# Kernel tuning notes

Measured on AMD Instinct MI355X. Metric: run time of the kernel, lower is better.

## Reference

```python
import jax, jax.numpy as jnp
import numpy as np

HIDDEN = 512
NUM_HEADS = 8
HEAD = HIDDEN // NUM_HEADS
TOP_K = 64
NEG = -1e9


def setup_inputs() -> dict:
    key = jax.random.key(0)
    ks = jax.random.split(key, 12)
    B, Q, S = 2, 2048, 4096
    sc = 0.02
    return {
        "main_input": jax.random.normal(ks[0], (B, Q, HIDDEN), jnp.float32),
        "side_input": jax.random.normal(ks[1], (S, HIDDEN), jnp.float32),
        "att_mask": jax.random.randint(ks[2], (B, Q, S), 0, 2, jnp.int32),
        "Wq": jax.random.normal(ks[3], (HIDDEN, HIDDEN), jnp.float32) * sc,
        "bq": jnp.zeros((HIDDEN,), jnp.float32),
        "Wk": jax.random.normal(ks[4], (HIDDEN, HIDDEN), jnp.float32) * sc,
        "bk": jnp.zeros((HIDDEN,), jnp.float32),
        "Wv": jax.random.normal(ks[5], (HIDDEN, HIDDEN), jnp.float32) * sc,
        "bv": jnp.zeros((HIDDEN,), jnp.float32),
        "Wo": jax.random.normal(ks[6], (HIDDEN, HIDDEN), jnp.float32) * sc,
        "bo": jnp.zeros((HIDDEN,), jnp.float32),
    }


def reference(main_input, side_input, att_mask, Wq, bq, Wk, bk, Wv, bv, Wo, bo):
    B, Qlen, _ = main_input.shape
    S = side_input.shape[0]
    # multi-head projections; side K/V shared across the whole batch
    q = (main_input @ Wq + bq).reshape(B, Qlen, NUM_HEADS, HEAD)
    k = (side_input @ Wk + bk).reshape(S, NUM_HEADS, HEAD)
    v = (side_input @ Wv + bv).reshape(S, NUM_HEADS, HEAD)
    # scores: [B, H, Q, S]
    scores = jnp.einsum("bqhd,khd->bhqk", q, k) / jnp.sqrt(jnp.asarray(HEAD, q.dtype))
    # attention mask (0 = masked)
    mask = att_mask[:, None, :, :].astype(scores.dtype)  # [B,1,Q,S]
    scores = scores + (1.0 - mask) * NEG
    # top-k restriction: keep only the TOP_K largest scores per query row
    thresh = jax.lax.top_k(scores, TOP_K)[0][..., -1:]  # kth largest
    scores = jnp.where(scores >= thresh, scores, NEG)
    probs = jax.nn.softmax(scores, axis=-1)
    ctx = jnp.einsum("bhqk,khd->bqhd", probs, v).reshape(B, Qlen, HIDDEN)
    return ctx @ Wo + bo
```

## Files before the change

### kernel.cpp

```cpp
#include <hip/hip_runtime.h>
#include <stdint.h>

typedef uint32_t u32;
typedef unsigned long long u64;

#define NEGV (-1e9f)
#define NCAND 16
#define LISTCAP 256

__device__ __forceinline__ u32 f2ord(float f) {
  u32 x = __float_as_uint(f);
  return (x & 0x80000000u) ? ~x : (x | 0x80000000u);
}
__device__ __forceinline__ float ord2f(u32 u) {
  u32 x = (u & 0x80000000u) ? (u ^ 0x80000000u) : ~u;
  return __uint_as_float(x);
}

__global__ __launch_bounds__(256)
void pack_mask(const int* __restrict__ mask, u64* __restrict__ mbits) {
  int w = blockIdx.x * 256 + threadIdx.x;
  const int4* p = (const int4*)(mask + (size_t)w * 64);
  u64 bits = 0;
#pragma unroll
  for (int j = 0; j < 16; ++j) {
    int4 m = p[j];
    if (m.x) bits |= 1ull << (j * 4 + 0);
    if (m.y) bits |= 1ull << (j * 4 + 1);
    if (m.z) bits |= 1ull << (j * 4 + 2);
    if (m.w) bits |= 1ull << (j * 4 + 3);
  }
  mbits[w] = bits;
}

__global__ __launch_bounds__(256)
void gemm_bias(const float* __restrict__ A, const float* __restrict__ W,
               const float* __restrict__ bias, float* __restrict__ C) {
  __shared__ float As[16][68];
  __shared__ float Bs[16][64];
  const int tid = threadIdx.x;
  const int tx = tid & 15, ty = tid >> 4;
  const int n0 = blockIdx.x << 6, m0 = blockIdx.y << 6;
  float c[4][4] = {};
  for (int k0 = 0; k0 < 512; k0 += 16) {
    {
      const int row = tid >> 2, kp = (tid & 3) << 2;
      float4 av = *(const float4*)&A[(size_t)(m0 + row) * 512 + k0 + kp];
      As[kp + 0][row] = av.x;
      As[kp + 1][row] = av.y;
      As[kp + 2][row] = av.z;
      As[kp + 3][row] = av.w;
      const int kk = tid >> 4, np = (tid & 15) << 2;
      *(float4*)&Bs[kk][np] = *(const float4*)&W[(size_t)(k0 + kk) * 512 + n0 + np];
    }
    __syncthreads();
#pragma unroll
    for (int kk = 0; kk < 16; ++kk) {
      float4 a = *(const float4*)&As[kk][ty << 2];
      float4 b = *(const float4*)&Bs[kk][tx << 2];
      c[0][0] += a.x * b.x; c[0][1] += a.x * b.y; c[0][2] += a.x * b.z; c[0][3] += a.x * b.w;
      c[1][0] += a.y * b.x; c[1][1] += a.y * b.y; c[1][2] += a.y * b.z; c[1][3] += a.y * b.w;
      c[2][0] += a.z * b.x; c[2][1] += a.z * b.y; c[2][2] += a.z * b.z; c[2][3] += a.z * b.w;
      c[3][0] += a.w * b.x; c[3][1] += a.w * b.y; c[3][2] += a.w * b.z; c[3][3] += a.w * b.w;
    }
    __syncthreads();
  }
  float4 bv = *(const float4*)&bias[n0 + (tx << 2)];
#pragma unroll
  for (int i = 0; i < 4; ++i) {
    float4 o;
    o.x = c[i][0] + bv.x; o.y = c[i][1] + bv.y;
    o.z = c[i][2] + bv.z; o.w = c[i][3] + bv.w;
    *(float4*)&C[(size_t)(m0 + (ty << 2) + i) * 512 + n0 + (tx << 2)] = o;
  }
}

__global__ __launch_bounds__(256)
void gemm_bias_T(const float* __restrict__ A, const float* __restrict__ W,
                 const float* __restrict__ bias, float* __restrict__ CT, int qsh) {
  __shared__ float As[16][68];
  __shared__ float Bs[16][64];
  const int tid = threadIdx.x;
  const int tx = tid & 15, ty = tid >> 4;
  const int n0 = blockIdx.x << 6, m0 = blockIdx.y << 6;
  float c[4][4] = {};
  for (int k0 = 0; k0 < 512; k0 += 16) {
    {
      const int row = tid >> 2, kp = (tid & 3) << 2;
      float4 av = *(const float4*)&A[(size_t)(m0 + row) * 512 + k0 + kp];
      As[kp + 0][row] = av.x;
      As[kp + 1][row] = av.y;
      As[kp + 2][row] = av.z;
      As[kp + 3][row] = av.w;
      const int kk = tid >> 4, np = (tid & 15) << 2;
      *(float4*)&Bs[kk][np] = *(const float4*)&W[(size_t)(k0 + kk) * 512 + n0 + np];
    }
    __syncthreads();
#pragma unroll
    for (int kk = 0; kk < 16; ++kk) {
      float4 a = *(const float4*)&As[kk][ty << 2];
      float4 b = *(const float4*)&Bs[kk][tx << 2];
      c[0][0] += a.x * b.x; c[0][1] += a.x * b.y; c[0][2] += a.x * b.z; c[0][3] += a.x * b.w;
      c[1][0] += a.y * b.x; c[1][1] += a.y * b.y; c[1][2] += a.y * b.z; c[1][3] += a.y * b.w;
      c[2][0] += a.z * b.x; c[2][1] += a.z * b.y; c[2][2] += a.z * b.z; c[2][3] += a.z * b.w;
      c[3][0] += a.w * b.x; c[3][1] += a.w * b.y; c[3][2] += a.w * b.z; c[3][3] += a.w * b.w;
    }
    __syncthreads();
  }
  float4 bv = *(const float4*)&bias[n0 + (tx << 2)];
  float bvv[4] = {bv.x, bv.y, bv.z, bv.w};
  const int qlen = 1 << qsh;
  const int qmask = qlen - 1;
#pragma unroll
  for (int i = 0; i < 4; ++i) {
#pragma unroll
    for (int j = 0; j < 4; ++j) {
      float val = c[i][j] + bvv[j];
      int m = m0 + (ty << 2) + i;
      int n = n0 + (tx << 2) + j;
      int h = n >> 6, d = n & 63;
      int bb = m >> qsh, q = m & qmask;
      CT[(((size_t)bb * 8 + h) * 64 + d) * qlen + q] = val;
    }
  }
}

__global__ __launch_bounds__(256)
void score_kernel(const float* __restrict__ qT, const float* __restrict__ kT,
                  const u64* __restrict__ mbits, float* __restrict__ sbuf,
                  float* __restrict__ segmax, int sl0) {
  __shared__ float Qs[64][128];
  __shared__ float Ks[64][128];
  const int sl = sl0 + blockIdx.z;
  const int b = sl >> 3, h = sl & 7;
  const int s0 = blockIdx.x << 7, q0 = blockIdx.y << 7;
  const int tid = threadIdx.x;
  const float* qbase = qT + (size_t)sl * 64 * 2048 + q0;
  const float* kbase = kT + (size_t)h * 64 * 4096 + s0;
  float4* Qf = (float4*)&Qs[0][0];
  float4* Kf = (float4*)&Ks[0][0];
#pragma unroll
  for (int u = 0; u < 8; ++u) {
    int i = (u << 8) + tid;
    int row = i >> 5, col = (i & 31) << 2;
    Qf[i] = *(const float4*)(qbase + (size_t)row * 2048 + col);
    Kf[i] = *(const float4*)(kbase + (size_t)row * 4096 + col);
  }
  __syncthreads();
  const int tx = tid & 15, ty = tid >> 4;
  float c[8][8] = {};
#pragma unroll 4
  for (int g = 0; g < 16; ++g) {
    const int kk = g << 2;
    float qa[8][4], kb[8][4];
#pragma unroll
    for (int t = 0; t < 4; ++t) {
#pragma unroll
      for (int i = 0; i < 8; ++i) qa[i][t] = Qs[kk + t][(ty << 3) + i];
#pragma unroll
      for (int j = 0; j < 4; ++j) {
        kb[j][t]     = Ks[kk + t][(tx << 2) + j];
        kb[4 + j][t] = Ks[kk + t][64 + (tx << 2) + j];
      }
    }
#pragma unroll
    for (int i = 0; i < 8; ++i)
#pragma unroll
      for (int j = 0; j < 8; ++j)
        c[i][j] += qa[i][0] * kb[j][0] + qa[i][1] * kb[j][1]
                 + qa[i][2] * kb[j][2] + qa[i][3] * kb[j][3];
  }
  float* srow = sbuf + ((size_t)blockIdx.z * 2048 + q0) * 4096 + s0;
  const u64* mrow = mbits + ((size_t)(b * 2048 + q0)) * 64 + (s0 >> 6);
#pragma unroll
  for (int i = 0; i < 8; ++i) {
    const int row = (ty << 3) + i;
    u64 wA = mrow[(size_t)row * 64];
    u64 wB = mrow[(size_t)row * 64 + 1];
    float4 o0, o1;
    o0.x = ((wA >> ((tx << 2) + 0)) & 1) ? c[i][0] * 0.125f : NEGV;
    o0.y = ((wA >> ((tx << 2) + 1)) & 1) ? c[i][1] * 0.125f : NEGV;
    o0.z = ((wA >> ((tx << 2) + 2)) & 1) ? c[i][2] * 0.125f : NEGV;
    o0.w = ((wA >> ((tx << 2) + 3)) & 1) ? c[i][3] * 0.125f : NEGV;
    o1.x = ((wB >> ((tx << 2) + 0)) & 1) ? c[i][4] * 0.125f : NEGV;
    o1.y = ((wB >> ((tx << 2) + 1)) & 1) ? c[i][5] * 0.125f : NEGV;
    o1.z = ((wB >> ((tx << 2) + 2)) & 1) ? c[i][6] * 0.125f : NEGV;
    o1.w = ((wB >> ((tx << 2) + 3)) & 1) ? c[i][7] * 0.125f : NEGV;
    *(float4*)&srow[(size_t)row * 4096 + (tx << 2)] = o0;
    *(float4*)&srow[(size_t)row * 4096 + 64 + (tx << 2)] = o1;
    float m0 = fmaxf(fmaxf(o0.x, o0.y), fmaxf(o0.z, o0.w));
    float m1 = fmaxf(fmaxf(o1.x, o1.y), fmaxf(o1.z, o1.w));
#pragma unroll
    for (int off = 4; off; off >>= 1) {
      m0 = fmaxf(m0, __shfl_xor(m0, off, 64));
      m1 = fmaxf(m1, __shfl_xor(m1, off, 64));
    }
    if ((tx & 7) == 0) {
      size_t sg = ((size_t)blockIdx.z * 2048 + q0 + row) * 128 + (s0 >> 5) + (tx >> 3);
      segmax[sg] = m0;
      segmax[sg + 2] = m1;
    }
  }
}

__global__ __launch_bounds__(256)
void topk_ctx_kernel(const float* __restrict__ sbuf, const float* __restrict__ segmax,
                     const float* __restrict__ vbuf, float* __restrict__ ctxbuf,
                     int sl0) {
  const int sl = sl0 + blockIdx.y;
  const int b = sl >> 3, h = sl & 7;
  const int w = threadIdx.x >> 6, lane = threadIdx.x & 63;
  const int qi = (blockIdx.x << 2) + w;
  __shared__ u64 cand_lds[4][NCAND][64];
  u64* list = &cand_lds[w][0][0];
  const u64 lmask_lt = (1ull << lane) - 1ull;
  const u32 ordneg = f2ord(NEGV);

  const float* srow = sbuf + ((size_t)blockIdx.y * 2048 + qi) * 4096;

  float2 smv = *(const float2*)(segmax + ((size_t)blockIdx.y * 2048 + qi) * 128 + (lane << 1));
  u32 so0 = f2ord(smv.x), so1 = f2ord(smv.y);
  u32 mxo = so0 > so1 ? so0 : so1;
  u32 mno = so0 < so1 ? so0 : so1;
#pragma unroll
  for (int off = 32; off; off >>= 1) {
    u32 a = (u32)__shfl_xor((int)mxo, off, 64);
    u32 c = (u32)__shfl_xor((int)mno, off, 64);
    mxo = a > mxo ? a : mxo;
    mno = c < mno ? c : mno;
  }
  const float fm = ord2f(mxo);
  {
    u32 lo = mno, hi = mxo + 1;
    while (hi - lo > 1) {
      u32 mid = lo + ((hi - lo) >> 1);
      int c = __popcll(__ballot(so0 >= mid)) + __popcll(__ballot(so1 >= mid));
      if (c >= 64) lo = mid; else hi = mid;
    }
    mno = lo;
  }
  const u32 ordT = mno;
  const float Tf = ord2f(ordT);

  int cnt = 0;
  const float* lbase = srow + (lane << 6);
#pragma unroll
  for (int reg = 0; reg < 2; ++reg) {
    bool active = (reg == 0) ? (smv.x >= Tf) : (smv.y >= Tf);
    if (active) {
      const float* rb = lbase + (reg << 5);
      float4 v0 = *(const float4*)(rb + 0);
      float4 v1 = *(const float4*)(rb + 4);
      float4 v2 = *(const float4*)(rb + 8);
      float4 v3 = *(const float4*)(rb + 12);
      float4 v4 = *(const float4*)(rb + 16);
      float4 v5 = *(const float4*)(rb + 20);
      float4 v6 = *(const float4*)(rb + 24);
      float4 v7 = *(const float4*)(rb + 28);
      float xs[32] = {v0.x, v0.y, v0.z, v0.w, v1.x, v1.y, v1.z, v1.w,
                      v2.x, v2.y, v2.z, v2.w, v3.x, v3.y, v3.z, v3.w,
                      v4.x, v4.y, v4.z, v4.w, v5.x, v5.y, v5.z, v5.w,
                      v6.x, v6.y, v6.z, v6.w, v7.x, v7.y, v7.z, v7.w};
#pragma unroll
      for (int cc = 0; cc < 32; ++cc) {
        if (xs[cc] >= Tf) {
          if (cnt < NCAND) {
            int sidx = (lane << 6) + (reg << 5) + cc;
            cand_lds[w][cnt][lane] = ((u64)f2ord(xs[cc]) << 32) | (u32)sidx;
          }
          cnt++;
        }
      }
    }
  }
  const bool fb = (__ballot(cnt > NCAND) != 0ull);

  float esum = 0.f;
  int nsel = 0;
  bool meanpath = false;

  if (!fb) {
    u32 co[NCAND];
#pragma unroll
    for (int j = 0; j < NCAND; ++j)
      co[j] = (j < cnt) ? ((const u32*)&cand_lds[w][j][lane])[1] : 0u;
    u32 lo = ordT, hi = mxo + 1;
    while (hi - lo > 1) {
      u32 mid = lo + ((hi - lo) >> 1);
      int c = 0;
#pragma unroll
      for (int j = 0; j < NCAND; ++j)
        c += __popcll(__ballot(co[j] >= mid));
      if (c >= 64) lo = mid; else hi = mid;
    }
    int base = 0;
#pragma unroll
    for (int j = 0; j < NCAND; ++j) {
      bool pred = (j < cnt) && (co[j] >= lo);
      u64 m = __ballot(pred);
      int ofs = base + __popcll(m & lmask_lt);
      if (pred && ofs < LISTCAP) {
        u64 cj = cand_lds[w][j][lane];
        float ev = __expf(ord2f((u32)(cj >> 32)) - fm);
        list[ofs] = ((u64)((u32)cj) << 32) | (u64)__float_as_uint(ev);
        esum += ev;
      }
      base += (int)__popcll(m);
    }
    nsel = base < LISTCAP ? base : LISTCAP;
  } else {
    u32 lo = ordT, hi = mxo + 1;
    while (hi - lo > 1) {
      u32 mid = lo + ((hi - lo) >> 1);
      float midf = ord2f(mid);
      int c = 0;
      for (int j = 0; j < 16; ++j) {
        float4 v = *(const float4*)(srow + (j << 8) + (lane << 2));
        c += __popcll(__ballot(v.x >= midf)) + __popcll(__ballot(v.y >= midf)) +
             __popcll(__ballot(v.z >= midf)) + __popcll(__ballot(v.w >= midf));
      }
      if (c >= 64) lo = mid; else hi = mid;
    }
    const float thrf = ord2f(lo);
    int base = 0;
    for (int j = 0; j < 16; ++j) {
      float4 v = *(const float4*)(srow + (j << 8) + (lane << 2));
      float xs[4] = {v.x, v.y, v.z, v.w};
#pragma unroll
      for (int cpos = 0; cpos < 4; ++cpos) {
        float x = xs[cpos];
        bool pred = (x >= thrf) && (x != NEGV);
        u64 m = __ballot(pred);
        int ofs = base + __popcll(m & lmask_lt);
        if (pred && ofs < LISTCAP) {
          int sidx = (j << 8) + (lane << 2) + cpos;
          float ev = __expf(x - fm);
          list[ofs] = ((u64)(u32)sidx << 32) | (u64)__float_as_uint(ev);
          esum += ev;
        }
        base += (int)__popcll(m);
      }
    }
    nsel = base < LISTCAP ? base : LISTCAP;
    if (base == 0) meanpath = true;
  }

#pragma unroll
  for (int off = 32; off; off >>= 1) esum += __shfl_xor(esum, off, 64);
  const float* vb = vbuf + h * 64 + lane;
  float outv;
  if (!meanpath) {
    const float rs = 1.0f / esum;
    int pad = (8 - (nsel & 7)) & 7;
    if (lane < pad && nsel + lane < LISTCAP) list[nsel + lane] = 0;
    int n8 = nsel + pad;
    if (n8 > LISTCAP) n8 = LISTCAP;
    float a0 = 0.f, a1 = 0.f, a2 = 0.f, a3 = 0.f;
    float a4 = 0.f, a5 = 0.f, a6 = 0.f, a7 = 0.f;
    for (int g = 0; g < n8; g += 8) {
      u64 p0 = list[g + 0], p1 = list[g + 1], p2 = list[g + 2], p3 = list[g + 3];
      u64 p4 = list[g + 4], p5 = list[g + 5], p6 = list[g + 6], p7 = list[g + 7];
      a0 += __uint_as_float((u32)p0) * vb[(size_t)(p0 >> 32) * 512];
      a1 += __uint_as_float((u32)p1) * vb[(size_t)(p1 >> 32) * 512];
      a2 += __uint_as_float((u32)p2) * vb[(size_t)(p2 >> 32) * 512];
      a3 += __uint_as_float((u32)p3) * vb[(size_t)(p3 >> 32) * 512];
      a4 += __uint_as_float((u32)p4) * vb[(size_t)(p4 >> 32) * 512];
      a5 += __uint_as_float((u32)p5) * vb[(size_t)(p5 >> 32) * 512];
      a6 += __uint_as_float((u32)p6) * vb[(size_t)(p6 >> 32) * 512];
      a7 += __uint_as_float((u32)p7) * vb[(size_t)(p7 >> 32) * 512];
    }
    outv = (((a0 + a1) + (a2 + a3)) + ((a4 + a5) + (a6 + a7))) * rs;
  } else {
    float acc = 0.f;
    for (int s = 0; s < 4096; ++s) acc += vb[(size_t)s * 512];
    outv = acc * (1.0f / 4096.0f);
  }
  ctxbuf[((size_t)(b * 2048 + qi)) * 512 + h * 64 + lane] = outv;
}

extern "C" void kernel_launch(void* const* d_in, const int* in_sizes, int n_in,
                              void* d_out, int out_size, void* d_ws, size_t ws_size,
                              hipStream_t stream) {
  const float* main_in = (const float*)d_in[0];
  const float* side_in = (const float*)d_in[1];
  const int*   mask    = (const int*)d_in[2];
  const float* Wq = (const float*)d_in[3];
  const float* bq = (const float*)d_in[4];
  const float* Wk = (const float*)d_in[5];
  const float* bk = (const float*)d_in[6];
  const float* Wv = (const float*)d_in[7];
  const float* bv = (const float*)d_in[8];
  const float* Wo = (const float*)d_in[9];
  const float* bo = (const float*)d_in[10];
  float* out = (float*)d_out;

  char* ws = (char*)d_ws;
  float* qT   = (float*)(ws);
  float* kT   = (float*)(ws + ((size_t)8 << 20));
  float* vbuf = (float*)(ws + ((size_t)16 << 20));
  float* ctxb = (float*)(ws + ((size_t)24 << 20));
  u64* mbits  = (u64*)(ws + ((size_t)32 << 20));
  const size_t base = (size_t)34 << 20;
  const size_t sliceb = (size_t)2048 * 4096 * 4;
  const size_t segb   = (size_t)2048 * 128 * 4;
  const size_t per = sliceb + segb;

  int nz = 1;
  if (ws_size > base + per) {
    size_t m = (ws_size - base) / per;
    nz = (int)(m > 4 ? 4 : m);
  }
  float* sbuf = (float*)(ws + base);
  float* smax = (float*)(ws + base + (size_t)nz * sliceb);

  pack_mask<<<1024, 256, 0, stream>>>(mask, mbits);
  gemm_bias_T<<<dim3(8, 64), 256, 0, stream>>>(main_in, Wq, bq, qT, 11);
  gemm_bias_T<<<dim3(8, 64), 256, 0, stream>>>(side_in, Wk, bk, kT, 12);
  gemm_bias  <<<dim3(8, 64), 256, 0, stream>>>(side_in, Wv, bv, vbuf);

  for (int sl0 = 0; sl0 < 16; sl0 += nz) {
    int z = nz < (16 - sl0) ? nz : (16 - sl0);
    score_kernel   <<<dim3(32, 16, z), 256, 0, stream>>>(qT, kT, mbits, sbuf, smax, sl0);
    topk_ctx_kernel<<<dim3(512, z), 256, 0, stream>>>(sbuf, smax, vbuf, ctxb, sl0);
  }

  gemm_bias<<<dim3(8, 64), 256, 0, stream>>>(ctxb, Wo, bo, out);
}
```

Baseline: 749.3 us.

## Compute scores with split-fp16 MFMA and refine top-k candidates exactly

Replaces the scalar fp32 score GEMM with MFMA f16 instructions, using a hi/lo fp16 split of Q and K (three MFMA passes) to approximate fp32 precision. The projection GEMM now emits the fp16 hi/lo planes plus a row-major fp32 copy, and score tiles are staged into LDS with direct global-to-LDS loads and an XOR swizzle. Because the MFMA scores are approximate, the top-k threshold is loosened by a small delta, and the candidates are rescored exactly with a double-precision dot product before selection. This adds extra projection output traffic and per-candidate gathers of K rows in the top-k kernel, in exchange for much cheaper score computation.

```diff
diff --git a/kernel.cpp b/kernel.cpp
--- a/kernel.cpp
+++ b/kernel.cpp
@@ -7,6 +7,12 @@
 #define NEGV (-1e9f)
 #define NCAND 16
 #define LISTCAP 256
+#define RSCALE 2048.0f
+#define RINV   (1.0f / 2048.0f)
+#define DELTA  4e-3f
+
+typedef __attribute__((ext_vector_type(8))) _Float16 half8;
+typedef __attribute__((ext_vector_type(4))) float f32x4;
 
 __device__ __forceinline__ u32 f2ord(float f) {
   u32 x = __float_as_uint(f);
@@ -15,6 +21,12 @@
 __device__ __forceinline__ float ord2f(u32 u) {
   u32 x = (u & 0x80000000u) ? (u ^ 0x80000000u) : ~u;
   return __uint_as_float(x);
+}
+
+__device__ __forceinline__ void gl_lds16(const unsigned short* g, unsigned short* l) {
+  __builtin_amdgcn_global_load_lds(
+      (const __attribute__((address_space(1))) u32*)g,
+      (__attribute__((address_space(3))) u32*)l, 16, 0, 0);
 }
 
 __global__ __launch_bounds__(256)
@@ -76,8 +88,10 @@
 }
 
 __global__ __launch_bounds__(256)
-void gemm_bias_T(const float* __restrict__ A, const float* __restrict__ W,
-                 const float* __restrict__ bias, float* __restrict__ CT, int qsh) {
+void gemm_bias_split(const float* __restrict__ A, const float* __restrict__ W,
+                     const float* __restrict__ bias,
+                     unsigned short* __restrict__ Ph, unsigned short* __restrict__ Pl,
+                     float* __restrict__ Pf, int qsh) {
   __shared__ float As[16][68];
   __shared__ float Bs[16][64];
   const int tid = threadIdx.x;
@@ -109,114 +123,175 @@
   }
   float4 bv = *(const float4*)&bias[n0 + (tx << 2)];
   float bvv[4] = {bv.x, bv.y, bv.z, bv.w};
-  const int qlen = 1 << qsh;
-  const int qmask = qlen - 1;
+  const int h = blockIdx.x;
+  const int QL = 1 << qsh;
 #pragma unroll
   for (int i = 0; i < 4; ++i) {
+    const int m = m0 + (ty << 2) + i;
+    const size_t base =
+        (((size_t)((m >> qsh) * 8 + h)) * QL + (m & (QL - 1))) * 64 + (tx << 2);
+    u64 hb = 0, lb = 0;
+    float fv[4];
 #pragma unroll
     for (int j = 0; j < 4; ++j) {
       float val = c[i][j] + bvv[j];
-      int m = m0 + (ty << 2) + i;
-      int n = n0 + (tx << 2) + j;
-      int h = n >> 6, d = n & 63;
-      int bb = m >> qsh, q = m & qmask;
-      CT[(((size_t)bb * 8 + h) * 64 + d) * qlen + q] = val;
-    }
-  }
-}
-
-__global__ __launch_bounds__(256)
-void score_kernel(const float* __restrict__ qT, const float* __restrict__ kT,
-                  const u64* __restrict__ mbits, float* __restrict__ sbuf,
-                  float* __restrict__ segmax, int sl0) {
-  __shared__ float Qs[64][128];
-  __shared__ float Ks[64][128];
+      fv[j] = val;
+      union { _Float16 f; unsigned short u; } ch, cl;
+      ch.f = (_Float16)val;
+      float hf = (float)ch.f;
+      cl.f = (_Float16)((val - hf) * RSCALE);
+      hb |= (u64)ch.u << (16 * j);
+      lb |= (u64)cl.u << (16 * j);
+    }
+    float4 fo;
+    fo.x = fv[0]; fo.y = fv[1]; fo.z = fv[2]; fo.w = fv[3];
+    *(u64*)&Ph[base] = hb;
+    *(u64*)&Pl[base] = lb;
+    *(float4*)&Pf[base] = fo;
+  }
+}
+
+__global__ __launch_bounds__(256, 2)
+void score_mfma(const unsigned short* __restrict__ qh, const unsigned short* __restrict__ ql,
+                const unsigned short* __restrict__ kh, const unsigned short* __restrict__ kl,
+                const u64* __restrict__ mbits, float* __restrict__ sbuf,
+                float* __restrict__ segmax, int sl0) {
+  __shared__ alignas(16) unsigned short lds[4][128][64];
   const int sl = sl0 + blockIdx.z;
   const int b = sl >> 3, h = sl & 7;
   const int s0 = blockIdx.x << 7, q0 = blockIdx.y << 7;
   const int tid = threadIdx.x;
-  const float* qbase = qT + (size_t)sl * 64 * 2048 + q0;
-  const float* kbase = kT + (size_t)h * 64 * 4096 + s0;
-  float4* Qf = (float4*)&Qs[0][0];
-  float4* Kf = (float4*)&Ks[0][0];
-#pragma unroll
-  for (int u = 0; u < 8; ++u) {
-    int i = (u << 8) + tid;
-    int row = i >> 5, col = (i & 31) << 2;
-    Qf[i] = *(const float4*)(qbase + (size_t)row * 2048 + col);
-    Kf[i] = *(const float4*)(kbase + (size_t)row * 4096 + col);
+  const int lane = tid & 63, w = tid >> 6;
+
+  const unsigned short* q0p = qh + ((size_t)sl * 2048 + q0) * 64;
+  const unsigned short* q1p = ql + ((size_t)sl * 2048 + q0) * 64;
+  const unsigned short* k0p = kh + ((size_t)h * 4096 + s0) * 64;
+  const unsigned short* k1p = kl + ((size_t)h * 4096 + s0) * 64;
+
+  {
+    const int r8 = lane >> 3, pc = lane & 7;
+#pragma unroll
+    for (int u = 0; u < 4; ++u) {
+      const int row = (w << 5) + (u << 3) + r8;
+      const size_t src = (size_t)row * 64 + (size_t)((pc ^ (row & 7)) << 3);
+      unsigned short* d0 = &lds[0][(w << 5) + (u << 3)][0];
+      unsigned short* d1 = &lds[1][(w << 5) + (u << 3)][0];
+      unsigned short* d2 = &lds[2][(w << 5) + (u << 3)][0];
+      unsigned short* d3 = &lds[3][(w << 5) + (u << 3)][0];
+      gl_lds16(q0p + src, d0);
+      gl_lds16(q1p + src, d1);
+      gl_lds16(k0p + src, d2);
+      gl_lds16(k1p + src, d3);
+    }
   }
   __syncthreads();
-  const int tx = tid & 15, ty = tid >> 4;
-  float c[8][8] = {};
-#pragma unroll 4
-  for (int g = 0; g < 16; ++g) {
-    const int kk = g << 2;
-    float qa[8][4], kb[8][4];
-#pragma unroll
-    for (int t = 0; t < 4; ++t) {
-#pragma unroll
-      for (int i = 0; i < 8; ++i) qa[i][t] = Qs[kk + t][(ty << 3) + i];
-#pragma unroll
-      for (int j = 0; j < 4; ++j) {
-        kb[j][t]     = Ks[kk + t][(tx << 2) + j];
-        kb[4 + j][t] = Ks[kk + t][64 + (tx << 2) + j];
-      }
-    }
-#pragma unroll
-    for (int i = 0; i < 8; ++i)
-#pragma unroll
-      for (int j = 0; j < 8; ++j)
-        c[i][j] += qa[i][0] * kb[j][0] + qa[i][1] * kb[j][1]
-                 + qa[i][2] * kb[j][2] + qa[i][3] * kb[j][3];
-  }
-  float* srow = sbuf + ((size_t)blockIdx.z * 2048 + q0) * 4096 + s0;
-  const u64* mrow = mbits + ((size_t)(b * 2048 + q0)) * 64 + (s0 >> 6);
-#pragma unroll
-  for (int i = 0; i < 8; ++i) {
-    const int row = (ty << 3) + i;
-    u64 wA = mrow[(size_t)row * 64];
-    u64 wB = mrow[(size_t)row * 64 + 1];
-    float4 o0, o1;
-    o0.x = ((wA >> ((tx << 2) + 0)) & 1) ? c[i][0] * 0.125f : NEGV;
-    o0.y = ((wA >> ((tx << 2) + 1)) & 1) ? c[i][1] * 0.125f : NEGV;
-    o0.z = ((wA >> ((tx << 2) + 2)) & 1) ? c[i][2] * 0.125f : NEGV;
-    o0.w = ((wA >> ((tx << 2) + 3)) & 1) ? c[i][3] * 0.125f : NEGV;
-    o1.x = ((wB >> ((tx << 2) + 0)) & 1) ? c[i][4] * 0.125f : NEGV;
-    o1.y = ((wB >> ((tx << 2) + 1)) & 1) ? c[i][5] * 0.125f : NEGV;
-    o1.z = ((wB >> ((tx << 2) + 2)) & 1) ? c[i][6] * 0.125f : NEGV;
-    o1.w = ((wB >> ((tx << 2) + 3)) & 1) ? c[i][7] * 0.125f : NEGV;
-    *(float4*)&srow[(size_t)row * 4096 + (tx << 2)] = o0;
-    *(float4*)&srow[(size_t)row * 4096 + 64 + (tx << 2)] = o1;
-    float m0 = fmaxf(fmaxf(o0.x, o0.y), fmaxf(o0.z, o0.w));
-    float m1 = fmaxf(fmaxf(o1.x, o1.y), fmaxf(o1.z, o1.w));
-#pragma unroll
-    for (int off = 4; off; off >>= 1) {
-      m0 = fmaxf(m0, __shfl_xor(m0, off, 64));
-      m1 = fmaxf(m1, __shfl_xor(m1, off, 64));
-    }
-    if ((tx & 7) == 0) {
-      size_t sg = ((size_t)blockIdx.z * 2048 + q0 + row) * 128 + (s0 >> 5) + (tx >> 3);
-      segmax[sg] = m0;
-      segmax[sg + 2] = m1;
+
+  const int r16 = lane & 15, g = lane >> 4;
+  const int qw = (w >> 1) << 6;
+  const int sw = (w & 1) << 6;
+
+  f32x4 accB[4][4] = {};
+  f32x4 accS[4][4] = {};
+  half8 aH[2][4], bH[2][4], tX[2][4];
+
+#define FRAG(p, rowbase, c_)                                                     \
+  (*(const half8*)&lds[p][(rowbase) + r16][(((c_) ^ (((rowbase) + r16) & 7)) << 3)])
+
+#pragma unroll
+  for (int ks = 0; ks < 2; ++ks)
+#pragma unroll
+    for (int i = 0; i < 4; ++i) {
+      aH[ks][i] = FRAG(0, qw + (i << 4), g + (ks << 2));
+      bH[ks][i] = FRAG(2, sw + (i << 4), g + (ks << 2));
+    }
+#pragma unroll
+  for (int ks = 0; ks < 2; ++ks)
+#pragma unroll
+    for (int i = 0; i < 4; ++i)
+#pragma unroll
+      for (int j = 0; j < 4; ++j)
+        accB[i][j] = __builtin_amdgcn_mfma_f32_16x16x32_f16(aH[ks][i], bH[ks][j], accB[i][j], 0, 0, 0);
+#pragma unroll
+  for (int ks = 0; ks < 2; ++ks)
+#pragma unroll
+    for (int i = 0; i < 4; ++i)
+      tX[ks][i] = FRAG(3, sw + (i << 4), g + (ks << 2));
+#pragma unroll
+  for (int ks = 0; ks < 2; ++ks)
+#pragma unroll
+    for (int i = 0; i < 4; ++i)
+#pragma unroll
+      for (int j = 0; j < 4; ++j)
+        accS[i][j] = __builtin_amdgcn_mfma_f32_16x16x32_f16(aH[ks][i], tX[ks][j], accS[i][j], 0, 0, 0);
+#pragma unroll
+  for (int ks = 0; ks < 2; ++ks)
+#pragma unroll
+    for (int i = 0; i < 4; ++i)
+      tX[ks][i] = FRAG(1, qw + (i << 4), g + (ks << 2));
+#pragma unroll
+  for (int ks = 0; ks < 2; ++ks)
+#pragma unroll
+    for (int i = 0; i < 4; ++i)
+#pragma unroll
+      for (int j = 0; j < 4; ++j)
+        accS[i][j] = __builtin_amdgcn_mfma_f32_16x16x32_f16(tX[ks][i], bH[ks][j], accS[i][j], 0, 0, 0);
+#undef FRAG
+
+  const int sword = (s0 + sw) >> 6;
+  const int sseg = (s0 + sw) >> 5;
+#pragma unroll
+  for (int i = 0; i < 4; ++i) {
+#pragma unroll
+    for (int r = 0; r < 4; ++r) {
+      const int qg = q0 + qw + (i << 4) + (g << 2) + r;
+      const u64 wm = mbits[((size_t)b * 2048 + qg) * 64 + sword];
+      float s0v = (accB[i][0][r] + accS[i][0][r] * RINV) * 0.125f;
+      float s1v = (accB[i][1][r] + accS[i][1][r] * RINV) * 0.125f;
+      float s2v = (accB[i][2][r] + accS[i][2][r] * RINV) * 0.125f;
+      float s3v = (accB[i][3][r] + accS[i][3][r] * RINV) * 0.125f;
+      float v0 = ((wm >> (0 + r16)) & 1)  ? s0v : NEGV;
+      float v1 = ((wm >> (16 + r16)) & 1) ? s1v : NEGV;
+      float v2 = ((wm >> (32 + r16)) & 1) ? s2v : NEGV;
+      float v3 = ((wm >> (48 + r16)) & 1) ? s3v : NEGV;
+      float* rowp = sbuf + ((size_t)blockIdx.z * 2048 + qg) * 4096 + s0 + sw;
+      rowp[r16] = v0;
+      rowp[16 + r16] = v1;
+      rowp[32 + r16] = v2;
+      rowp[48 + r16] = v3;
+      float m01 = fmaxf(v0, v1), m23 = fmaxf(v2, v3);
+#pragma unroll
+      for (int off = 8; off; off >>= 1) {
+        m01 = fmaxf(m01, __shfl_xor(m01, off, 64));
+        m23 = fmaxf(m23, __shfl_xor(m23, off, 64));
+      }
+      if (r16 == 0) {
+        size_t sg = ((size_t)blockIdx.z * 2048 + qg) * 128 + sseg;
+        segmax[sg] = m01;
+        segmax[sg + 1] = m23;
+      }
     }
   }
 }
 
 __global__ __launch_bounds__(256)
 void topk_ctx_kernel(const float* __restrict__ sbuf, const float* __restrict__ segmax,
-                     const float* __restrict__ vbuf, float* __restrict__ ctxbuf,
-                     int sl0) {
+                     const float* __restrict__ vbuf,
+                     const float* __restrict__ qF, const float* __restrict__ kF,
+                     float* __restrict__ ctxbuf, int sl0) {
   const int sl = sl0 + blockIdx.y;
   const int b = sl >> 3, h = sl & 7;
   const int w = threadIdx.x >> 6, lane = threadIdx.x & 63;
   const int qi = (blockIdx.x << 2) + w;
   __shared__ u64 cand_lds[4][NCAND][64];
-  u64* list = &cand_lds[w][0][0];
+  __shared__ u64 list_lds[4][LISTCAP];
+  __shared__ alignas(16) float qrow[4][64];
+  u64* list = &list_lds[w][0];
   const u64 lmask_lt = (1ull << lane) - 1ull;
-  const u32 ordneg = f2ord(NEGV);
 
   const float* srow = sbuf + ((size_t)blockIdx.y * 2048 + qi) * 4096;
+
+  qrow[w][lane] = qF[((size_t)sl * 2048 + qi) * 64 + lane];
+  __syncthreads();
 
   float2 smv = *(const float2*)(segmax + ((size_t)blockIdx.y * 2048 + qi) * 128 + (lane << 1));
   u32 so0 = f2ord(smv.x), so1 = f2ord(smv.y);
@@ -240,13 +315,13 @@
     mno = lo;
   }
   const u32 ordT = mno;
-  const float Tf = ord2f(ordT);
+  const float TfD = ord2f(ordT) - DELTA;
 
   int cnt = 0;
   const float* lbase = srow + (lane << 6);
 #pragma unroll
   for (int reg = 0; reg < 2; ++reg) {
-    bool active = (reg == 0) ? (smv.x >= Tf) : (smv.y >= Tf);
+    bool active = (reg == 0) ? (smv.x >= TfD) : (smv.y >= TfD);
     if (active) {
       const float* rb = lbase + (reg << 5);
       float4 v0 = *(const float4*)(rb + 0);
@@ -263,7 +338,7 @@
                       v6.x, v6.y, v6.z, v6.w, v7.x, v7.y, v7.z, v7.w};
 #pragma unroll
       for (int cc = 0; cc < 32; ++cc) {
-        if (xs[cc] >= Tf) {
+        if (xs[cc] >= TfD) {
           if (cnt < NCAND) {
             int sidx = (lane << 6) + (reg << 5) + cc;
             cand_lds[w][cnt][lane] = ((u64)f2ord(xs[cc]) << 32) | (u32)sidx;
@@ -280,11 +355,42 @@
   bool meanpath = false;
 
   if (!fb) {
+    const float* kb = kF + (size_t)h * 4096 * 64;
     u32 co[NCAND];
-#pragma unroll
-    for (int j = 0; j < NCAND; ++j)
-      co[j] = (j < cnt) ? ((const u32*)&cand_lds[w][j][lane])[1] : 0u;
-    u32 lo = ordT, hi = mxo + 1;
+    u32 mymax = 0u, mymin = 0xFFFFFFFFu;
+#pragma unroll
+    for (int j = 0; j < NCAND; ++j) {
+      if (j < cnt) {
+        const u32 sidx = (u32)cand_lds[w][j][lane];
+        const float* kr = kb + (size_t)sidx * 64;
+        double acc = 0.0;
+#pragma unroll 4
+        for (int dq = 0; dq < 16; ++dq) {
+          float4 kv = *(const float4*)(kr + (dq << 2));
+          float4 qv = *(const float4*)&qrow[w][dq << 2];
+          acc += (double)kv.x * (double)qv.x;
+          acc += (double)kv.y * (double)qv.y;
+          acc += (double)kv.z * (double)qv.z;
+          acc += (double)kv.w * (double)qv.w;
+        }
+        float s = (float)(acc * 0.125);
+        u32 o = f2ord(s);
+        co[j] = o;
+        mymax = o > mymax ? o : mymax;
+        mymin = o < mymin ? o : mymin;
+      } else {
+        co[j] = 0u;
+      }
+    }
+#pragma unroll
+    for (int off = 32; off; off >>= 1) {
+      u32 a = (u32)__shfl_xor((int)mymax, off, 64);
+      u32 c = (u32)__shfl_xor((int)mymin, off, 64);
+      mymax = a > mymax ? a : mymax;
+      mymin = c < mymin ? c : mymin;
+    }
+    const float fmr = ord2f(mymax);
+    u32 lo = mymin, hi = mymax + 1;
     while (hi - lo > 1) {
       u32 mid = lo + ((hi - lo) >> 1);
       int c = 0;
@@ -300,9 +406,9 @@
       u64 m = __ballot(pred);
       int ofs = base + __popcll(m & lmask_lt);
       if (pred && ofs < LISTCAP) {
-        u64 cj = cand_lds[w][j][lane];
-        float ev = __expf(ord2f((u32)(cj >> 32)) - fm);
-        list[ofs] = ((u64)((u32)cj) << 32) | (u64)__float_as_uint(ev);
+        u32 sidx = (u32)cand_lds[w][j][lane];
+        float ev = __expf(ord2f(co[j]) - fmr);
+        list[ofs] = ((u64)sidx << 32) | (u64)__float_as_uint(ev);
         esum += ev;
       }
       base += (int)__popcll(m);
@@ -395,33 +501,38 @@
   float* out = (float*)d_out;
 
   char* ws = (char*)d_ws;
-  float* qT   = (float*)(ws);
-  float* kT   = (float*)(ws + ((size_t)8 << 20));
-  float* vbuf = (float*)(ws + ((size_t)16 << 20));
-  float* ctxb = (float*)(ws + ((size_t)24 << 20));
+  float* vbuf = (float*)(ws);
+  float* ctxb = (float*)(ws + ((size_t)8 << 20));
+  unsigned short* qhp = (unsigned short*)(ws + ((size_t)16 << 20));
+  unsigned short* qlp = (unsigned short*)(ws + ((size_t)20 << 20));
+  unsigned short* khp = (unsigned short*)(ws + ((size_t)24 << 20));
+  unsigned short* klp = (unsigned short*)(ws + ((size_t)28 << 20));
   u64* mbits  = (u64*)(ws + ((size_t)32 << 20));
-  const size_t base = (size_t)34 << 20;
+  float* qFp  = (float*)(ws + ((size_t)34 << 20));
+  float* kFp  = (float*)(ws + ((size_t)42 << 20));
+  const size_t base = (size_t)50 << 20;
   const size_t sliceb = (size_t)2048 * 4096 * 4;
   const size_t segb   = (size_t)2048 * 128 * 4;
   const size_t per = sliceb + segb;
 
   int nz = 1;
-  if (ws_size > base + per) {
+  if (ws_size > base) {
     size_t m = (ws_size - base) / per;
-    nz = (int)(m > 4 ? 4 : m);
+    if (m >= 1) nz = (int)(m > 4 ? 4 : m);
   }
   float* sbuf = (float*)(ws + base);
   float* smax = (float*)(ws + base + (size_t)nz * sliceb);
 
   pack_mask<<<1024, 256, 0, stream>>>(mask, mbits);
-  gemm_bias_T<<<dim3(8, 64), 256, 0, stream>>>(main_in, Wq, bq, qT, 11);
-  gemm_bias_T<<<dim3(8, 64), 256, 0, stream>>>(side_in, Wk, bk, kT, 12);
+  gemm_bias_split<<<dim3(8, 64), 256, 0, stream>>>(main_in, Wq, bq, qhp, qlp, qFp, 11);
+  gemm_bias_split<<<dim3(8, 64), 256, 0, stream>>>(side_in, Wk, bk, khp, klp, kFp, 12);
   gemm_bias  <<<dim3(8, 64), 256, 0, stream>>>(side_in, Wv, bv, vbuf);
 
   for (int sl0 = 0; sl0 < 16; sl0 += nz) {
     int z = nz < (16 - sl0) ? nz : (16 - sl0);
-    score_kernel   <<<dim3(32, 16, z), 256, 0, stream>>>(qT, kT, mbits, sbuf, smax, sl0);
-    topk_ctx_kernel<<<dim3(512, z), 256, 0, stream>>>(sbuf, smax, vbuf, ctxb, sl0);
+    score_mfma     <<<dim3(32, 16, z), 256, 0, stream>>>(qhp, qlp, khp, klp, mbits, sbuf, smax, sl0);
+    topk_ctx_kernel<<<dim3(512, z), 256, 0, stream>>>(sbuf, smax, vbuf,
+                                                      qFp, kFp, ctxb, sl0);
   }
 
   gemm_bias<<<dim3(8, 64), 256, 0, stream>>>(ctxb, Wo, bo, out);
```

Result: slower. 826.8 us (+10.3%).
